# Kernel tuning notes

Measured on AMD Instinct MI355X. Metric: run time of the kernel, lower is better.

## Reference

```python
import jax, jax.numpy as jnp
import numpy as np

PAD = 4
KERNEL = 1
MAX_DISP = 4
STRIDE1 = 1
STRIDE2 = 1


def setup_inputs() -> dict:
    key = jax.random.key(0)
    k1, k2 = jax.random.split(key)
    B, C, H, W = 16, 128, 96, 160
    input1 = jax.random.normal(k1, (B, C, H, W), dtype=jnp.float32)
    input2 = jax.random.normal(k2, (B, C, H, W), dtype=jnp.float32)
    return {"input1": input1, "input2": input2}


def _correlation(input1, input2):
    # FlowNet-style patch cross-correlation (corr_multiply=1).
    # Output[b, d, y, x] = sum_{c, patch} I1[b,c,patch(y,x)] * I2[b,c,patch(y+dy,x+dx)] / (K*K*C)
    B, C, H, W = input1.shape
    kr = (KERNEL - 1) // 2  # kernel radius (0 for KERNEL=1)
    p1 = jnp.pad(input1, ((0, 0), (0, 0), (PAD, PAD), (PAD, PAD)))
    p2 = jnp.pad(input2, ((0, 0), (0, 0), (PAD, PAD), (PAD, PAD)))
    norm = jnp.float32(KERNEL * KERNEL * C)
    outs = []
    for dy in range(-MAX_DISP, MAX_DISP + 1, STRIDE2):
        for dx in range(-MAX_DISP, MAX_DISP + 1, STRIDE2):
            acc = jnp.zeros((B, H, W), dtype=input1.dtype)
            for ki in range(-kr, kr + 1):
                for kj in range(-kr, kr + 1):
                    a = p1[:, :, PAD + ki:PAD + ki + H, PAD + kj:PAD + kj + W]
                    b = p2[:, :, PAD + ki + dy:PAD + ki + dy + H,
                              PAD + kj + dx:PAD + kj + dx + W]
                    acc = acc + jnp.sum(a * b, axis=1)
            outs.append(acc / norm)
    return jnp.stack(outs, axis=1)  # [B, (2*md/s2+1)^2, H, W]


def reference(input1, input2):
    return _correlation(input1, input2)
```

## Files before the change

kernel.cpp:

```cpp
#include <hip/hip_runtime.h>
#include <stdint.h>

typedef __bf16 bf16;
typedef __attribute__((ext_vector_type(4))) __bf16 bf16x4;
typedef __attribute__((ext_vector_type(8))) __bf16 bf16x8;
typedef __attribute__((ext_vector_type(4))) float f32x4;
typedef __attribute__((ext_vector_type(4))) unsigned int u32x4;

#define W_ 160
#define H_ 96
#define C_ 128
#define B_ 16
#define HW_ (H_ * W_)
#define NXT 10
#define NYB4 24
#define NBLK (B_ * NYB4 * NXT)
#define SLICEB 10240
#define YB 40960
#define ROWSB 2048
#define CHB (12 * ROWSB)
#define WSSTR 1312

__device__ float g_zero[16];

__device__ __forceinline__ void g2l16(const void* g, void* l) {
    __builtin_amdgcn_global_load_lds(
        (const __attribute__((address_space(1))) void*)g,
        (__attribute__((address_space(3))) void*)l, 16, 0, 0);
}

__global__ __launch_bounds__(256) void t2_kernel(const float* __restrict__ in2,
                                                 char* __restrict__ o) {
    __shared__ __align__(16) char T[40960];
    const int L   = blockIdx.x;
    const int tid = threadIdx.x;
    const float* src = in2 + (size_t)(L / H_) * C_ * HW_ + (size_t)(L % H_) * W_;
    char* dst = o + (size_t)L * YB;
    const float SC = 1.0f / 128.0f;
#pragma unroll
    for (int rd = 0; rd < 5; ++rd) {
        const int s  = rd * 256 + tid;
        const int cq = s / 40;
        const int x4 = s - cq * 40;
        const float* p = src + (size_t)(4 * cq) * HW_ + 4 * x4;
        const float4 v0 = *(const float4*)(p);
        const float4 v1 = *(const float4*)(p + HW_);
        const float4 v2 = *(const float4*)(p + 2 * HW_);
        const float4 v3 = *(const float4*)(p + 3 * HW_);
        const int oq = cq >> 1, half = cq & 1;
#pragma unroll
        for (int xj = 0; xj < 4; ++xj) {
            const int x   = 4 * x4 + xj;
            const int pos = oq ^ ((x >> 2) & 15);
            bf16x4 pk;
            pk[0] = (bf16)(((const float*)&v0)[xj] * SC);
            pk[1] = (bf16)(((const float*)&v1)[xj] * SC);
            pk[2] = (bf16)(((const float*)&v2)[xj] * SC);
            pk[3] = (bf16)(((const float*)&v3)[xj] * SC);
            *(bf16x4*)(T + x * 256 + pos * 16 + half * 8) = pk;
        }
    }
    __syncthreads();
#pragma unroll
    for (int wr = 0; wr < 10; ++wr) {
        const int s2  = wr * 256 + tid;
        const int ck  = s2 / 640;
        const int r   = s2 - ck * 640;
        const int x   = r >> 2;
        const int gsw = r & 3;
        const int gg  = gsw ^ ((x >> 1) & 3);
        const int oo  = ck * 4 + gg;
        const int pos = oo ^ ((x >> 2) & 15);
        const u32x4 v = *(const u32x4*)(T + x * 256 + pos * 16);
        *(u32x4*)(dst + (size_t)s2 * 16) = v;
    }
}

__global__ __launch_bounds__(256, 3) void corr_mfma4(const float* __restrict__ in1,
                                                     const char* __restrict__ in2t,
                                                     float* __restrict__ out) {
    __shared__ __align__(16) char Bsm[2 * CHB];

    const int L   = ((int)blockIdx.x & 7) * (NBLK / 8) + ((int)blockIdx.x >> 3);
    const int b   = L / (NYB4 * NXT);
    const int rem = L % (NYB4 * NXT);
    const int yb  = rem / NXT;
    const int xt  = rem % NXT;
    const int x0  = xt * 16, y0 = yb * 4;

    const int tid  = threadIdx.x;
    const int wv   = __builtin_amdgcn_readfirstlane(tid >> 6);
    const int lane = tid & 63;
    const int n    = lane & 15;
    const int g    = lane >> 4;
    const int y    = y0 + wv;

    const char* i2tb = in2t + (size_t)b * (H_ * YB);

    const char* srow[6];
    bool stgv[6];
#pragma unroll
    for (int rd = 0; rd < 6; ++rd) {
        const int s   = rd * 256 + tid;
        const int row = s >> 7;
        const int sl  = s & 127;
        const int gy  = y0 - 4 + row;
        const int x   = x0 - 4 + (sl >> 2);
        stgv[rd] = (sl < 96) && ((unsigned)gy < (unsigned)H_) && ((unsigned)x < (unsigned)W_);
        const int gy_c = min(max(gy, 0), H_ - 1);
        const int ofs  = max((x0 - 4) * 64 + sl * 16, 0);
        srow[rd] = i2tb + (size_t)gy_c * YB + ofs;
    }

#define STAGE(CK, DST)                                                        \
    {                                                                         \
        _Pragma("unroll")                                                     \
        for (int rd = 0; rd < 6; ++rd)                                        \
            g2l16(stgv[rd] ? (const void*)(srow[rd] + (CK) * SLICEB)          \
                           : (const void*)g_zero,                             \
                  (void*)((DST) + rd * 4096 + tid * 16));                     \
    }

    STAGE(0, Bsm);

    const float* abase = in1 + (size_t)b * C_ * HW_ + (size_t)y * W_ + (x0 + n);
    float a_raw[32];
#pragma unroll
    for (int i = 0; i < 32; ++i)
        a_raw[i] = abase[(size_t)((i >> 3) * 32 + g * 8 + (i & 7)) * HW_];
    bf16x8 afrag[4];
#pragma unroll
    for (int ck = 0; ck < 4; ++ck)
#pragma unroll
        for (int j = 0; j < 8; ++j)
            afrag[ck][j] = (bf16)a_raw[ck * 8 + j];

    int rboff[2];
#pragma unroll
    for (int t = 0; t < 2; ++t) {
        const int xl = n + 16 * t;
        const int sw = g ^ (((xl + 12) >> 1) & 3);
        rboff[t] = (xl * 4 + sw) * 16;
    }

    f32x4 acc[9][2];
#pragma unroll
    for (int dyi = 0; dyi < 9; ++dyi)
#pragma unroll
        for (int t = 0; t < 2; ++t)
            acc[dyi][t] = (f32x4){0.f, 0.f, 0.f, 0.f};

    __syncthreads();

#pragma unroll
    for (int ck = 0; ck < 4; ++ck) {
        const char* cbuf = Bsm + (ck & 1) * CHB;
        if (ck < 3) STAGE(ck + 1, Bsm + ((ck + 1) & 1) * CHB);
#pragma unroll
        for (int dyi = 0; dyi < 9; ++dyi) {
            const int rowoff = (wv + dyi) * ROWSB;
#pragma unroll
            for (int t = 0; t < 2; ++t) {
                const bf16x8 bfrag = *(const bf16x8*)(cbuf + rowoff + rboff[t]);
                acc[dyi][t] = __builtin_amdgcn_mfma_f32_16x16x32_bf16(
                    afrag[ck], bfrag, acc[dyi][t], 0, 0, 0);
            }
        }
        if (ck < 3) __syncthreads();
    }
#undef STAGE

    float* wsw = (float*)Bsm + wv * WSSTR;
#pragma unroll
    for (int dyi = 0; dyi < 9; ++dyi)
#pragma unroll
        for (int t = 0; t < 2; ++t)
#pragma unroll
            for (int rr = 0; rr < 4; ++rr) {
                const int m = 4 * g + rr;
                const int d = n + 16 * t - m;
                if ((unsigned)d <= 8u)
                    wsw[(dyi * 9 + d) * 16 + m] = acc[dyi][t][rr];
            }
    __syncthreads();

    const int mm = lane & 15, rg = lane >> 4;
    const size_t ob = (size_t)(b * 81) * HW_ + (size_t)y * W_ + (x0 + mm);
#pragma unroll
    for (int q4 = 0; q4 < 20; ++q4) {
        const int rho = q4 * 4 + rg;
        out[ob + (size_t)rho * HW_] = wsw[rho * 16 + mm];
    }
    if (rg == 0)
        out[ob + (size_t)80 * HW_] = wsw[80 * 16 + mm];
}

extern "C" void kernel_launch(void* const* d_in, const int* in_sizes, int n_in,
                              void* d_out, int out_size, void* d_ws, size_t ws_size,
                              hipStream_t stream) {
    const float* in1 = (const float*)d_in[0];
    const float* in2 = (const float*)d_in[1];
    float* out = (float*)d_out;
    (void)in_sizes; (void)n_in; (void)out_size; (void)ws_size;
    char* in2t = (char*)d_ws;
    hipLaunchKernelGGL(t2_kernel, dim3(B_ * H_), dim3(256), 0, stream, in2, in2t);
    hipLaunchKernelGGL(corr_mfma4, dim3(NBLK), dim3(256), 0, stream, in1, in2t, out);
}
```

Before: 103.6 us.

## Triple-buffer input2 chunks with explicit vmcnt waits in correlation kernel

Moves the input1 fragment loads ahead of staging and waits for them, then issues three input2 channel chunks into a triple LDS buffer. Compute is interleaved with manual vmcnt-counted waits and raw barriers instead of a double-buffered loop with __syncthreads. The goal is more memory-latency overlap and fewer full syncs. In exchange, LDS per block grows and occupancy drops from 3 to 2 blocks per CU.

```diff
diff --git a/kernel.cpp b/kernel.cpp
--- a/kernel.cpp
+++ b/kernel.cpp
@@ -76,10 +76,10 @@
     }
 }
 
-__global__ __launch_bounds__(256, 3) void corr_mfma4(const float* __restrict__ in1,
+__global__ __launch_bounds__(256, 2) void corr_mfma5(const float* __restrict__ in1,
                                                      const char* __restrict__ in2t,
                                                      float* __restrict__ out) {
-    __shared__ __align__(16) char Bsm[2 * CHB];
+    __shared__ __align__(16) char Bsm[3 * CHB];
 
     const int L   = ((int)blockIdx.x & 7) * (NBLK / 8) + ((int)blockIdx.x >> 3);
     const int b   = L / (NYB4 * NXT);
@@ -112,6 +112,35 @@
         srow[rd] = i2tb + (size_t)gy_c * YB + ofs;
     }
 
+    const float* abase = in1 + (size_t)b * C_ * HW_ + (size_t)y * W_ + (x0 + n);
+    float a_raw[32];
+#pragma unroll
+    for (int i = 0; i < 32; ++i)
+        a_raw[i] = abase[(size_t)((i >> 3) * 32 + g * 8 + (i & 7)) * HW_];
+    bf16x8 afrag[4];
+#pragma unroll
+    for (int ck = 0; ck < 4; ++ck)
+#pragma unroll
+        for (int j = 0; j < 8; ++j)
+            afrag[ck][j] = (bf16)a_raw[ck * 8 + j];
+    asm volatile("s_waitcnt vmcnt(0)" ::: "memory");
+    __builtin_amdgcn_sched_barrier(0);
+
+    int rboff[2];
+#pragma unroll
+    for (int t = 0; t < 2; ++t) {
+        const int xl = n + 16 * t;
+        const int sw = g ^ (((xl + 12) >> 1) & 3);
+        rboff[t] = (xl * 4 + sw) * 16;
+    }
+
+    f32x4 acc[9][2];
+#pragma unroll
+    for (int dyi = 0; dyi < 9; ++dyi)
+#pragma unroll
+        for (int t = 0; t < 2; ++t)
+            acc[dyi][t] = (f32x4){0.f, 0.f, 0.f, 0.f};
+
 #define STAGE(CK, DST)                                                        \
     {                                                                         \
         _Pragma("unroll")                                                     \
@@ -120,55 +149,44 @@
                            : (const void*)g_zero,                             \
                   (void*)((DST) + rd * 4096 + tid * 16));                     \
     }
+#define WAITB(N)                                                              \
+    {                                                                         \
+        asm volatile("s_waitcnt vmcnt(" #N ")" ::: "memory");                 \
+        __builtin_amdgcn_s_barrier();                                         \
+        __builtin_amdgcn_sched_barrier(0);                                    \
+    }
+#define COMPUTE(CK, BUF)                                                      \
+    {                                                                         \
+        _Pragma("unroll")                                                     \
+        for (int dyi = 0; dyi < 9; ++dyi) {                                   \
+            const int rowoff = (wv + dyi) * ROWSB;                            \
+            _Pragma("unroll")                                                 \
+            for (int t = 0; t < 2; ++t) {                                     \
+                const bf16x8 bfrag =                                          \
+                    *(const bf16x8*)((BUF) + rowoff + rboff[t]);              \
+                acc[dyi][t] = __builtin_amdgcn_mfma_f32_16x16x32_bf16(        \
+                    afrag[CK], bfrag, acc[dyi][t], 0, 0, 0);                  \
+            }                                                                 \
+        }                                                                     \
+    }
 
     STAGE(0, Bsm);
-
-    const float* abase = in1 + (size_t)b * C_ * HW_ + (size_t)y * W_ + (x0 + n);
-    float a_raw[32];
-#pragma unroll
-    for (int i = 0; i < 32; ++i)
-        a_raw[i] = abase[(size_t)((i >> 3) * 32 + g * 8 + (i & 7)) * HW_];
-    bf16x8 afrag[4];
-#pragma unroll
-    for (int ck = 0; ck < 4; ++ck)
-#pragma unroll
-        for (int j = 0; j < 8; ++j)
-            afrag[ck][j] = (bf16)a_raw[ck * 8 + j];
-
-    int rboff[2];
-#pragma unroll
-    for (int t = 0; t < 2; ++t) {
-        const int xl = n + 16 * t;
-        const int sw = g ^ (((xl + 12) >> 1) & 3);
-        rboff[t] = (xl * 4 + sw) * 16;
-    }
-
-    f32x4 acc[9][2];
-#pragma unroll
-    for (int dyi = 0; dyi < 9; ++dyi)
-#pragma unroll
-        for (int t = 0; t < 2; ++t)
-            acc[dyi][t] = (f32x4){0.f, 0.f, 0.f, 0.f};
+    STAGE(1, Bsm + CHB);
+    STAGE(2, Bsm + 2 * CHB);
+    WAITB(12);
+    COMPUTE(0, Bsm);
+    WAITB(6);
+    STAGE(3, Bsm);
+    COMPUTE(1, Bsm + CHB);
+    WAITB(6);
+    COMPUTE(2, Bsm + 2 * CHB);
+    WAITB(0);
+    COMPUTE(3, Bsm);
+#undef STAGE
+#undef WAITB
+#undef COMPUTE
 
     __syncthreads();
-
-#pragma unroll
-    for (int ck = 0; ck < 4; ++ck) {
-        const char* cbuf = Bsm + (ck & 1) * CHB;
-        if (ck < 3) STAGE(ck + 1, Bsm + ((ck + 1) & 1) * CHB);
-#pragma unroll
-        for (int dyi = 0; dyi < 9; ++dyi) {
-            const int rowoff = (wv + dyi) * ROWSB;
-#pragma unroll
-            for (int t = 0; t < 2; ++t) {
-                const bf16x8 bfrag = *(const bf16x8*)(cbuf + rowoff + rboff[t]);
-                acc[dyi][t] = __builtin_amdgcn_mfma_f32_16x16x32_bf16(
-                    afrag[ck], bfrag, acc[dyi][t], 0, 0, 0);
-            }
-        }
-        if (ck < 3) __syncthreads();
-    }
-#undef STAGE
 
     float* wsw = (float*)Bsm + wv * WSSTR;
 #pragma unroll
@@ -204,5 +222,5 @@
     (void)in_sizes; (void)n_in; (void)out_size; (void)ws_size;
     char* in2t = (char*)d_ws;
     hipLaunchKernelGGL(t2_kernel, dim3(B_ * H_), dim3(256), 0, stream, in2, in2t);
-    hipLaunchKernelGGL(corr_mfma4, dim3(NBLK), dim3(256), 0, stream, in1, in2t, out);
-}
+    hipLaunchKernelGGL(corr_mfma5, dim3(NBLK), dim3(256), 0, stream, in1, in2t, out);
+}
```

After: 109.6 us. +5.8%, slower.
